# Kernel tuning notes

Measured on AMD Instinct MI355X. Metric: run time of the kernel, lower is better.

Reference implementation:

```python
import jax, jax.numpy as jnp
import numpy as np

EMBED = 1024
HEADS = 16
HEAD_DIM = EMBED // HEADS
SCALE = HEAD_DIM ** -0.5


def setup_inputs() -> dict:
    key = jax.random.key(0)
    ks = jax.random.split(key, 9)
    B, N = 2, 2048
    std = EMBED ** -0.5
    return {
        "query": jax.random.normal(ks[0], (B, N, EMBED), jnp.float32),
        "key": jax.random.normal(ks[1], (B, N, EMBED), jnp.float32),
        "value": jax.random.normal(ks[2], (B, N, EMBED), jnp.float32),
        # torch nn.Linear weights are [out, in]; y = x @ W.T + b
        "Wq": jax.random.normal(ks[3], (EMBED, EMBED), jnp.float32) * std,
        "bq": jax.random.normal(ks[4], (EMBED,), jnp.float32) * 0.01,
        "Wk": jax.random.normal(ks[5], (EMBED, EMBED), jnp.float32) * std,
        "bk": jax.random.normal(ks[6], (EMBED,), jnp.float32) * 0.01,
        "Wv": jax.random.normal(ks[7], (EMBED, EMBED), jnp.float32) * std,
        "bv": jax.random.normal(ks[8], (EMBED,), jnp.float32) * 0.01,
    }


def reference(query, key, value, Wq, bq, Wk, bk, Wv, bv):
    B, NQ, _ = query.shape
    NK = key.shape[1]
    q = query @ Wq.T + bq  # [B, NQ, E]
    k = key @ Wk.T + bk    # [B, NK, E]
    v = value @ Wv.T + bv  # [B, NK, E]
    # split heads -> [B, H, N, Dh]
    q = q.reshape(B, NQ, HEADS, HEAD_DIM).transpose(0, 2, 1, 3)
    k = k.reshape(B, NK, HEADS, HEAD_DIM).transpose(0, 2, 1, 3)
    v = v.reshape(B, NK, HEADS, HEAD_DIM).transpose(0, 2, 1, 3)
    attn = jnp.einsum("bhqd,bhkd->bhqk", q, k) * SCALE  # [B, H, NQ, NK]
    attn = jax.nn.softmax(attn, axis=-1)
    out = jnp.einsum("bhqk,bhkd->bhqd", attn, v)  # [B, H, NQ, Dh]
    out = out.transpose(0, 2, 1, 3).reshape(B, NQ, EMBED)
    # o_proj is Identity (odim == embed_dim, o_proj=False); dropout is 0 (eval)
    return out
```

## Files before the change

### kernel.cpp

```cpp
#include <hip/hip_runtime.h>

#define EMB 1024
#define NSEQ 2048
#define NBATCH 2
#define NHEAD 16
#define DHEAD 64
#define QSCALE 0.18033688011112042f

typedef float f32x4 __attribute__((ext_vector_type(4)));
typedef short s16x8 __attribute__((ext_vector_type(8)));
typedef short s16x4 __attribute__((ext_vector_type(4)));

typedef __attribute__((address_space(3))) short lds_short;
typedef __attribute__((address_space(1))) const short glb_short;

__device__ __forceinline__ void gl_lds16(const short* g, short* l) {
    __builtin_amdgcn_global_load_lds((glb_short*)g, (lds_short*)l, 16, 0, 0);
}

__device__ __forceinline__ short bf16r(float f) {
    unsigned u = __float_as_uint(f);
    u += 0x7fffu + ((u >> 16) & 1u);
    return (short)(u >> 16);
}

__device__ __forceinline__ unsigned pkbf(float a, float b) {
#if defined(__has_builtin) && __has_builtin(__builtin_amdgcn_cvt_pk_bf16_f32)
    auto r = __builtin_amdgcn_cvt_pk_bf16_f32(a, b);
    unsigned u;
    __builtin_memcpy(&u, &r, 4);
    return u;
#else
    return ((unsigned)bf16r(a) & 0xffffu) | ((unsigned)bf16r(b) << 16);
#endif
}

__device__ __forceinline__ float fexp2(float x) {
#if defined(__has_builtin) && __has_builtin(__builtin_amdgcn_exp2f)
    return __builtin_amdgcn_exp2f(x);
#else
    return exp2f(x);
#endif
}

__global__ __launch_bounds__(256) void cvt6_kernel(
    const float* __restrict__ s0, const float* __restrict__ s1, const float* __restrict__ s2,
    const float* __restrict__ s3, const float* __restrict__ s4, const float* __restrict__ s5,
    short* __restrict__ d0, short* __restrict__ d1, short* __restrict__ d2,
    short* __restrict__ d3, short* __restrict__ d4, short* __restrict__ d5,
    int n0, int n1, int n2, int n3, int n4, int n5)
{
    const int seg = blockIdx.y;
    const float* s = (seg == 0) ? s0 : (seg == 1) ? s1 : (seg == 2) ? s2
                   : (seg == 3) ? s3 : (seg == 4) ? s4 : s5;
    short* d = (seg == 0) ? d0 : (seg == 1) ? d1 : (seg == 2) ? d2
             : (seg == 3) ? d3 : (seg == 4) ? d4 : d5;
    const int n = (seg == 0) ? n0 : (seg == 1) ? n1 : (seg == 2) ? n2
                : (seg == 3) ? n3 : (seg == 4) ? n4 : n5;

    const int i = (blockIdx.x * 256 + threadIdx.x) * 8;
    if (i >= n) return;
    float4 a = *(const float4*)(s + i);
    float4 b = *(const float4*)(s + i + 4);
    uint4 u = { pkbf(a.x, a.y), pkbf(a.z, a.w), pkbf(b.x, b.y), pkbf(b.z, b.w) };
    *(uint4*)(d + i) = u;
}

__global__ __launch_bounds__(256, 3) void proj2_kernel(
    const short* __restrict__ Xq, const short* __restrict__ Xk, const short* __restrict__ Xv,
    const short* __restrict__ Wq, const short* __restrict__ Wk, const short* __restrict__ Wv,
    const float* __restrict__ bq, const float* __restrict__ bk, const float* __restrict__ bv,
    short* __restrict__ Oq, short* __restrict__ Ok, short* __restrict__ Ov)
{
    const int z = blockIdx.z;
    const short* X    = (z == 0) ? Xq : (z == 1) ? Xk : Xv;
    const short* W    = (z == 0) ? Wq : (z == 1) ? Wk : Wv;
    const float* bias = (z == 0) ? bq : (z == 1) ? bk : bv;
    short* Out        = (z == 0) ? Oq : (z == 1) ? Ok : Ov;
    const float osc   = (z == 0) ? QSCALE : 1.0f;

    const int n0 = blockIdx.x * 128;
    const int m0 = blockIdx.y * 128;

    __shared__ __align__(16) short As[128 * 64];
    __shared__ __align__(16) short Bs[128 * 64];

    const int t    = threadIdx.x;
    const int lane = t & 63;
    const int wave = t >> 6;
    const int r    = lane & 15;
    const int quad = lane >> 4;
    const int wm   = (wave >> 1) * 64;
    const int wn   = (wave & 1) * 64;

    const int p0    = wave * 256 + lane;
    const int row0  = p0 >> 3;
    const int lc0   = (p0 & 7) ^ (row0 & 7);
    const short* gA = X + (size_t)(m0 + row0) * EMB + lc0 * 8;
    const short* gB = W + (size_t)(n0 + row0) * EMB + lc0 * 8;
    short* lA = As + p0 * 8;
    short* lB = Bs + p0 * 8;

    f32x4 acc[4][4];
#pragma unroll
    for (int i = 0; i < 4; ++i)
#pragma unroll
        for (int j = 0; j < 4; ++j)
#pragma unroll
            for (int v = 0; v < 4; ++v) acc[i][j][v] = 0.f;

    for (int k0 = 0; k0 < EMB; k0 += 64) {
#pragma unroll
        for (int i = 0; i < 4; ++i) {
            gl_lds16(gA + k0 + (size_t)8 * i * EMB, lA + i * 512);
            gl_lds16(gB + k0 + (size_t)8 * i * EMB, lB + i * 512);
        }
        __syncthreads();

#pragma unroll
        for (int ks = 0; ks < 2; ++ks) {
            const int fc = ((ks * 4 + quad) ^ (r & 7)) * 8;
            s16x8 af[4], bf[4];
#pragma unroll
            for (int i = 0; i < 4; ++i) af[i] = *(const s16x8*)&As[(wm + i * 16 + r) * 64 + fc];
#pragma unroll
            for (int j = 0; j < 4; ++j) bf[j] = *(const s16x8*)&Bs[(wn + j * 16 + r) * 64 + fc];
#pragma unroll
            for (int i = 0; i < 4; ++i)
#pragma unroll
                for (int j = 0; j < 4; ++j)
                    acc[i][j] = __builtin_amdgcn_mfma_f32_16x16x32_bf16(af[i], bf[j], acc[i][j], 0, 0, 0);
        }
        __syncthreads();
    }

    if (z != 2) {
#pragma unroll
        for (int j = 0; j < 4; ++j) {
            const int gn = n0 + wn + j * 16 + r;
            const float bb = bias[gn];
#pragma unroll
            for (int i = 0; i < 4; ++i)
#pragma unroll
                for (int reg = 0; reg < 4; ++reg) {
                    const int gm = m0 + wm + i * 16 + quad * 4 + reg;
                    Out[(size_t)gm * EMB + gn] = bf16r((acc[i][j][reg] + bb) * osc);
                }
        }
    } else {
#pragma unroll
        for (int j = 0; j < 4; ++j) {
            const int gn = n0 + wn + j * 16 + r;
            const float bb = bias[gn];
            const int hh = gn >> 6;
            const int dd = gn & 63;
#pragma unroll
            for (int i = 0; i < 4; ++i) {
                const int gm = m0 + wm + i * 16 + quad * 4;
                const int bi = gm >> 11;
                const int nn = gm & 2047;
                s16x4 pk;
#pragma unroll
                for (int reg = 0; reg < 4; ++reg) pk[reg] = bf16r(acc[i][j][reg] + bb);
                *(s16x4*)(Out + ((size_t)(bi * NHEAD + hh) * DHEAD + dd) * NSEQ + nn) = pk;
            }
        }
    }
}

__global__ __launch_bounds__(256) void proj_kernel(
    const float* __restrict__ Xq, const float* __restrict__ Xk, const float* __restrict__ Xv,
    const float* __restrict__ Wq, const float* __restrict__ Wk, const float* __restrict__ Wv,
    const float* __restrict__ bq, const float* __restrict__ bk, const float* __restrict__ bv,
    short* __restrict__ Oq, short* __restrict__ Ok, short* __restrict__ Ov)
{
    const int z = blockIdx.z;
    const float* X    = (z == 0) ? Xq : (z == 1) ? Xk : Xv;
    const float* W    = (z == 0) ? Wq : (z == 1) ? Wk : Wv;
    const float* bias = (z == 0) ? bq : (z == 1) ? bk : bv;
    short* Out        = (z == 0) ? Oq : (z == 1) ? Ok : Ov;
    const float osc   = (z == 0) ? QSCALE : 1.0f;

    const int n0 = blockIdx.x * 128;
    const int m0 = blockIdx.y * 128;

    __shared__ __align__(16) short As[128][40];
    __shared__ __align__(16) short Bs[128][40];

    const int t    = threadIdx.x;
    const int lane = t & 63;
    const int wave = t >> 6;
    const int r    = lane & 15;
    const int quad = lane >> 4;
    const int wm   = (wave >> 1) * 64;
    const int wn   = (wave & 1) * 64;

    const int srow = t >> 1;
    const int scol = (t & 1) << 4;

    f32x4 acc[4][4];
#pragma unroll
    for (int i = 0; i < 4; ++i)
#pragma unroll
        for (int j = 0; j < 4; ++j)
#pragma unroll
            for (int v = 0; v < 4; ++v) acc[i][j][v] = 0.f;

    for (int k0 = 0; k0 < EMB; k0 += 32) {
        const float4* xp = (const float4*)(X + (size_t)(m0 + srow) * EMB + k0 + scol);
        const float4* wp = (const float4*)(W + (size_t)(n0 + srow) * EMB + k0 + scol);
        float4 x0 = xp[0], x1 = xp[1], x2 = xp[2], x3 = xp[3];
        float4 w0 = wp[0], w1 = wp[1], w2 = wp[2], w3 = wp[3];
        uint4 a0 = { pkbf(x0.x, x0.y), pkbf(x0.z, x0.w), pkbf(x1.x, x1.y), pkbf(x1.z, x1.w) };
        uint4 a1 = { pkbf(x2.x, x2.y), pkbf(x2.z, x2.w), pkbf(x3.x, x3.y), pkbf(x3.z, x3.w) };
        uint4 b0 = { pkbf(w0.x, w0.y), pkbf(w0.z, w0.w), pkbf(w1.x, w1.y), pkbf(w1.z, w1.w) };
        uint4 b1 = { pkbf(w2.x, w2.y), pkbf(w2.z, w2.w), pkbf(w3.x, w3.y), pkbf(w3.z, w3.w) };
        *(uint4*)&As[srow][scol]     = a0;
        *(uint4*)&As[srow][scol + 8] = a1;
        *(uint4*)&Bs[srow][scol]     = b0;
        *(uint4*)&Bs[srow][scol + 8] = b1;
        __syncthreads();

        s16x8 af[4], bf[4];
#pragma unroll
        for (int i = 0; i < 4; ++i) af[i] = *(const s16x8*)&As[wm + i * 16 + r][quad * 8];
#pragma unroll
        for (int j = 0; j < 4; ++j) bf[j] = *(const s16x8*)&Bs[wn + j * 16 + r][quad * 8];
#pragma unroll
        for (int i = 0; i < 4; ++i)
#pragma unroll
            for (int j = 0; j < 4; ++j)
                acc[i][j] = __builtin_amdgcn_mfma_f32_16x16x32_bf16(af[i], bf[j], acc[i][j], 0, 0, 0);
        __syncthreads();
    }

#pragma unroll
    for (int j = 0; j < 4; ++j) {
        const int gn = n0 + wn + j * 16 + r;
        const float bb = bias[gn];
#pragma unroll
        for (int i = 0; i < 4; ++i)
#pragma unroll
            for (int reg = 0; reg < 4; ++reg) {
                const int gm = m0 + wm + i * 16 + quad * 4 + reg;
                Out[(size_t)gm * EMB + gn] = bf16r((acc[i][j][reg] + bb) * osc);
            }
    }
}

__global__ __launch_bounds__(256) void vtrans_kernel(
    const short* __restrict__ Vp, short* __restrict__ VT)
{
    const int n0 = blockIdx.x * 64;
    const int h  = blockIdx.y;
    const int b  = blockIdx.z;
    __shared__ __align__(16) short L[64][72];

    const int t  = threadIdx.x;
    const int rr = t >> 2;
    const int cc = (t & 3) * 16;

    const short* src = Vp + (size_t)(b * NSEQ + n0 + rr) * EMB + h * DHEAD + cc;
    s16x8 a = *(const s16x8*)src;
    s16x8 c = *(const s16x8*)(src + 8);
    *(s16x8*)&L[rr][cc]     = a;
    *(s16x8*)&L[rr][cc + 8] = c;
    __syncthreads();

    const int d  = t >> 2;
    const int c4 = (t & 3) * 16;
    short vals[16];
#pragma unroll
    for (int i = 0; i < 16; ++i) vals[i] = L[c4 + i][d];
    short* dst = VT + ((size_t)(b * NHEAD + h) * DHEAD + d) * NSEQ + n0 + c4;
    *(s16x8*)dst       = *(s16x8*)&vals[0];
    *(s16x8*)(dst + 8) = *(s16x8*)&vals[8];
}

__global__ __launch_bounds__(512, 4) void attn8_kernel(
    const short* __restrict__ Qp, const short* __restrict__ Kp,
    const short* __restrict__ VT, float* __restrict__ Out)
{
    const int qblk = blockIdx.x * 128;
    const int h    = blockIdx.y;
    const int b    = blockIdx.z;

    __shared__ __align__(16) char smem[34816];
    short* Ks   = (short*)smem;
    short* Vs   = (short*)smem + 128 * 64;
    float* fbuf = (float*)smem;

    const int t    = threadIdx.x;
    const int lane = t & 63;
    const int w    = t >> 6;
    const int r    = lane & 15;
    const int quad = lane >> 4;
    const int r7   = r & 7;

    const size_t rowbase = (size_t)b * NSEQ;
    const int    colbase = h * DHEAD;
    const size_t bh64    = (size_t)(b * NHEAD + h) * DHEAD;

    const short* qrow = Qp + (rowbase + qblk + w * 16 + r) * EMB + colbase;
    const s16x8 qf0 = *(const s16x8*)(qrow + quad * 8);
    const s16x8 qf1 = *(const s16x8*)(qrow + 32 + quad * 8);

    f32x4 accO[4];
#pragma unroll
    for (int dt = 0; dt < 4; ++dt)
#pragma unroll
        for (int v = 0; v < 4; ++v) accO[dt][v] = 0.f;
    float lsum0 = 0.f, lsum1 = 0.f;
    const f32x4 zf = {0.f, 0.f, 0.f, 0.f};

    const int krow = t >> 2;
    const int kc   = (t & 3) * 2;
    const int kcs  = kc ^ (krow & 7);
    const short* gK = Kp + (rowbase + krow) * EMB + colbase + kc * 8;
    short* lK0 = Ks + krow * 64 + kcs * 8;
    short* lK1 = Ks + krow * 64 + (kcs ^ 1) * 8;

    const int vrow = t >> 3;
    const int vc   = (t & 7) * 2;
    const int vcs  = vc ^ (vrow & 7);
    const short* gV = VT + (bh64 + vrow) * NSEQ + vc * 8;
    short* lV0 = Vs + vrow * 128 + vcs * 8;
    short* lV1 = Vs + vrow * 128 + (vcs ^ 1) * 8;

    const int kofs = (quad ^ r7) * 8;
    int vofs[4];
    {
        const int x4  = r7 & 4;
        const int qr3 = ((quad >> 1) ^ r7) & 3;
#pragma unroll
        for (int s = 0; s < 4; ++s)
            vofs[s] = ((((s << 2) ^ x4) | qr3) * 8) + (quad & 1) * 4;
    }

    s16x8 kr0 = *(const s16x8*)gK;
    s16x8 kr1 = *(const s16x8*)(gK + 8);
    s16x8 vr0 = *(const s16x8*)gV;
    s16x8 vr1 = *(const s16x8*)(gV + 8);
    const short* gKn = gK + (size_t)128 * EMB;
    const short* gVn = gV + 128;

    for (int kt = 0; kt < 16; ++kt) {
        *(s16x8*)lK0 = kr0;
        *(s16x8*)lK1 = kr1;
        *(s16x8*)lV0 = vr0;
        *(s16x8*)lV1 = vr1;
        __syncthreads();

        if (kt + 1 < 16) {
            kr0 = *(const s16x8*)gKn;
            kr1 = *(const s16x8*)(gKn + 8);
            vr0 = *(const s16x8*)gVn;
            vr1 = *(const s16x8*)(gVn + 8);
            gKn += (size_t)128 * EMB;
            gVn += 128;
        }

        s16x8 pf[4];
#pragma unroll
        for (int s = 0; s < 4; ++s) {
            const short* kb = Ks + (s * 32 + r) * 64;
            const s16x8 kf00 = *(const s16x8*)(kb + kofs);
            const s16x8 kf01 = *(const s16x8*)(kb + (kofs ^ 32));
            const s16x8 kf10 = *(const s16x8*)(kb + 16 * 64 + kofs);
            const s16x8 kf11 = *(const s16x8*)(kb + 16 * 64 + (kofs ^ 32));
            __builtin_amdgcn_s_setprio(1);
            f32x4 s0 = __builtin_amdgcn_mfma_f32_16x16x32_bf16(
                kf01, qf1, __builtin_amdgcn_mfma_f32_16x16x32_bf16(kf00, qf0, zf, 0, 0, 0), 0, 0, 0);
            f32x4 s1 = __builtin_amdgcn_mfma_f32_16x16x32_bf16(
                kf11, qf1, __builtin_amdgcn_mfma_f32_16x16x32_bf16(kf10, qf0, zf, 0, 0, 0), 0, 0, 0);
            __builtin_amdgcn_s_setprio(0);
            float p0[4], p1[4];
#pragma unroll
            for (int reg = 0; reg < 4; ++reg) {
                p0[reg] = fexp2(s0[reg]);
                p1[reg] = fexp2(s1[reg]);
                lsum0 += p0[reg];
                lsum1 += p1[reg];
            }
            uint4 uu = { pkbf(p0[0], p0[1]), pkbf(p0[2], p0[3]),
                         pkbf(p1[0], p1[1]), pkbf(p1[2], p1[3]) };
            __builtin_memcpy(&pf[s], &uu, 16);
        }

#pragma unroll
        for (int dt = 0; dt < 4; ++dt) {
            const short* vb = Vs + (dt * 16 + r) * 128;
            s16x8 vfl[4];
#pragma unroll
            for (int s = 0; s < 4; ++s) {
                s16x4 lo = *(const s16x4*)(vb + vofs[s]);
                s16x4 hi = *(const s16x4*)(vb + (vofs[s] ^ 16));
                vfl[s] = __builtin_shufflevector(lo, hi, 0, 1, 2, 3, 4, 5, 6, 7);
            }
            __builtin_amdgcn_s_setprio(1);
#pragma unroll
            for (int s = 0; s < 4; ++s)
                accO[dt] = __builtin_amdgcn_mfma_f32_16x16x32_bf16(vfl[s], pf[s], accO[dt], 0, 0, 0);
            __builtin_amdgcn_s_setprio(0);
        }
        __syncthreads();
    }

    float ls = lsum0 + lsum1;
    ls += __shfl_xor(ls, 16);
    ls += __shfl_xor(ls, 32);
    const float rl = 1.f / ls;

#pragma unroll
    for (int dt = 0; dt < 4; ++dt)
#pragma unroll
        for (int reg = 0; reg < 4; ++reg)
            fbuf[(w * 16 + r) * 68 + dt * 16 + quad * 4 + reg] = accO[dt][reg] * rl;
    __syncthreads();
    const int qi = t >> 2;
    const int c  = (t & 3) * 16;
    const float4* fp = (const float4*)&fbuf[qi * 68 + c];
    float4 o0 = fp[0], o1 = fp[1], o2 = fp[2], o3 = fp[3];
    float* op = Out + (rowbase + qblk + qi) * EMB + colbase + c;
    ((float4*)op)[0] = o0;
    ((float4*)op)[1] = o1;
    ((float4*)op)[2] = o2;
    ((float4*)op)[3] = o3;
}

__global__ __launch_bounds__(256) void attn_fb_kernel(
    const short* __restrict__ Qp, const short* __restrict__ Kp,
    const short* __restrict__ Vp, float* __restrict__ Out)
{
    const int qt = blockIdx.x;
    const int h  = blockIdx.y;
    const int b  = blockIdx.z;

    __shared__ __align__(16) short Ks[64][72];
    __shared__ __align__(16) short VsT[64][72];
    __shared__ __align__(16) short Ps[4][16][72];

    const int t    = threadIdx.x;
    const int lane = t & 63;
    const int w    = t >> 6;
    const int r    = lane & 15;
    const int quad = lane >> 4;

    const size_t rowbase = (size_t)b * NSEQ;
    const int colbase    = h * DHEAD;

    const short* Qr = Qp + (rowbase + qt * 64 + w * 16 + r) * EMB + colbase;
    const s16x8 qf0 = *(const s16x8*)(Qr + quad * 8);
    const s16x8 qf1 = *(const s16x8*)(Qr + 32 + quad * 8);

    float mrow[4], lrow[4];
    f32x4 accO[4];
#pragma unroll
    for (int i = 0; i < 4; ++i) {
        mrow[i] = -INFINITY;
        lrow[i] = 0.f;
#pragma unroll
        for (int v = 0; v < 4; ++v) accO[i][v] = 0.f;
    }

    const int srow = t >> 2;
    const int scol = (t & 3) << 4;

    for (int kt = 0; kt < 32; ++kt) {
        const short* Krow = Kp + (rowbase + kt * 64 + srow) * EMB + colbase + scol;
        const short* Vrow = Vp + (rowbase + kt * 64 + srow) * EMB + colbase + scol;
        s16x8 kv0 = *(const s16x8*)Krow;
        s16x8 kv1 = *(const s16x8*)(Krow + 8);
        s16x8 vv0 = *(const s16x8*)Vrow;
        s16x8 vv1 = *(const s16x8*)(Vrow + 8);
        *(s16x8*)&Ks[srow][scol]     = kv0;
        *(s16x8*)&Ks[srow][scol + 8] = kv1;
#pragma unroll
        for (int i = 0; i < 8; ++i) {
            VsT[scol + i][srow]     = vv0[i];
            VsT[scol + 8 + i][srow] = vv1[i];
        }
        __syncthreads();

        f32x4 sacc[4];
#pragma unroll
        for (int j = 0; j < 4; ++j) {
#pragma unroll
            for (int v = 0; v < 4; ++v) sacc[j][v] = 0.f;
            s16x8 kf0 = *(const s16x8*)&Ks[j * 16 + r][quad * 8];
            s16x8 kf1 = *(const s16x8*)&Ks[j * 16 + r][32 + quad * 8];
            sacc[j] = __builtin_amdgcn_mfma_f32_16x16x32_bf16(qf0, kf0, sacc[j], 0, 0, 0);
            sacc[j] = __builtin_amdgcn_mfma_f32_16x16x32_bf16(qf1, kf1, sacc[j], 0, 0, 0);
        }

        float rmax[4];
#pragma unroll
        for (int reg = 0; reg < 4; ++reg) rmax[reg] = -INFINITY;
#pragma unroll
        for (int j = 0; j < 4; ++j)
#pragma unroll
            for (int reg = 0; reg < 4; ++reg)
                rmax[reg] = fmaxf(rmax[reg], sacc[j][reg]);
#pragma unroll
        for (int reg = 0; reg < 4; ++reg) {
#pragma unroll
            for (int mask = 1; mask <= 8; mask <<= 1)
                rmax[reg] = fmaxf(rmax[reg], __shfl_xor(rmax[reg], mask, 64));
        }

        float alpha[4], rsum[4];
#pragma unroll
        for (int reg = 0; reg < 4; ++reg) {
            float mnew = fmaxf(mrow[reg], rmax[reg]);
            alpha[reg] = fexp2(mrow[reg] - mnew);
            mrow[reg]  = mnew;
            rsum[reg]  = 0.f;
        }

#pragma unroll
        for (int j = 0; j < 4; ++j)
#pragma unroll
            for (int reg = 0; reg < 4; ++reg) {
                float p = fexp2(sacc[j][reg] - mrow[reg]);
                rsum[reg] += p;
                Ps[w][quad * 4 + reg][j * 16 + r] = bf16r(p);
            }
#pragma unroll
        for (int reg = 0; reg < 4; ++reg) {
#pragma unroll
            for (int mask = 1; mask <= 8; mask <<= 1)
                rsum[reg] += __shfl_xor(rsum[reg], mask, 64);
            lrow[reg] = lrow[reg] * alpha[reg] + rsum[reg];
        }
#pragma unroll
        for (int j = 0; j < 4; ++j)
#pragma unroll
            for (int reg = 0; reg < 4; ++reg) accO[j][reg] *= alpha[reg];

#pragma unroll
        for (int s = 0; s < 2; ++s) {
            s16x8 pfr = *(const s16x8*)&Ps[w][r][s * 32 + quad * 8];
#pragma unroll
            for (int j = 0; j < 4; ++j) {
                s16x8 vfr = *(const s16x8*)&VsT[j * 16 + r][s * 32 + quad * 8];
                accO[j] = __builtin_amdgcn_mfma_f32_16x16x32_bf16(pfr, vfr, accO[j], 0, 0, 0);
            }
        }
        __syncthreads();
    }

#pragma unroll
    for (int j = 0; j < 4; ++j)
#pragma unroll
        for (int reg = 0; reg < 4; ++reg) {
            const int qrow = qt * 64 + w * 16 + quad * 4 + reg;
            Out[(rowbase + qrow) * EMB + colbase + j * 16 + r] = accO[j][reg] / lrow[reg];
        }
}

extern "C" void kernel_launch(void* const* d_in, const int* in_sizes, int n_in,
                              void* d_out, int out_size, void* d_ws, size_t ws_size,
                              hipStream_t stream) {
    const float* query = (const float*)d_in[0];
    const float* key   = (const float*)d_in[1];
    const float* value = (const float*)d_in[2];
    const float* Wq    = (const float*)d_in[3];
    const float* bq    = (const float*)d_in[4];
    const float* Wk    = (const float*)d_in[5];
    const float* bk    = (const float*)d_in[6];
    const float* Wv    = (const float*)d_in[7];
    const float* bv    = (const float*)d_in[8];
    float* out = (float*)d_out;

    const size_t XBUF = (size_t)NBATCH * NSEQ * EMB;
    const size_t WBUF = (size_t)EMB * EMB;

    short* Qb  = (short*)d_ws;
    short* Kb  = Qb + XBUF;
    short* Vb  = Kb + XBUF;
    short* VTb = Vb + XBUF;
    short* Xqb = VTb + XBUF;
    short* Xkb = Xqb + XBUF;
    short* Xvb = Xkb + XBUF;
    short* Wqb = Xvb + XBUF;
    short* Wkb = Wqb + WBUF;
    short* Wvb = Wkb + WBUF;

    const size_t need_full  = (7 * XBUF + 3 * WBUF) * sizeof(short);
    const size_t need_attn8 = 4 * XBUF * sizeof(short);

    if (ws_size >= need_full) {
        cvt6_kernel<<<dim3(2048, 6), 256, 0, stream>>>(
            query, key, value, Wq, Wk, Wv,
            Xqb, Xkb, Xvb, Wqb, Wkb, Wvb,
            (int)XBUF, (int)XBUF, (int)XBUF, (int)WBUF, (int)WBUF, (int)WBUF);
        proj2_kernel<<<dim3(EMB / 128, (NBATCH * NSEQ) / 128, 3), 256, 0, stream>>>(
            Xqb, Xkb, Xvb, Wqb, Wkb, Wvb, bq, bk, bv, Qb, Kb, VTb);
        attn8_kernel<<<dim3(NSEQ / 128, NHEAD, NBATCH), 512, 0, stream>>>(Qb, Kb, VTb, out);
    } else if (ws_size >= need_attn8) {
        proj_kernel<<<dim3(EMB / 128, (NBATCH * NSEQ) / 128, 3), 256, 0, stream>>>(
            query, key, value, Wq, Wk, Wv, bq, bk, bv, Qb, Kb, Vb);
        vtrans_kernel<<<dim3(NSEQ / 64, NHEAD, NBATCH), 256, 0, stream>>>(Vb, VTb);
        attn8_kernel<<<dim3(NSEQ / 128, NHEAD, NBATCH), 512, 0, stream>>>(Qb, Kb, VTb, out);
    } else {
        proj_kernel<<<dim3(EMB / 128, (NBATCH * NSEQ) / 128, 3), 256, 0, stream>>>(
            query, key, value, Wq, Wk, Wv, bq, bk, bv, Qb, Kb, Vb);
        attn_fb_kernel<<<dim3(NSEQ / 64, NHEAD, NBATCH), 256, 0, stream>>>(Qb, Kb, Vb, out);
    }
}
```

Measured before the change: 207.7 us.

## Split attention waves into two KV groups with 32-row query strips

The 8 waves are split into two groups, each handling half of a 256-key tile while every wave now computes 32 query rows instead of 16. The kernel loops 8 times over 256-key tiles instead of 16 times over 128-key tiles, halving the barriers and letting each K/V fragment read from LDS feed two query strips. The two groups' partial outputs and row sums are merged through shared memory at the end. In exchange, LDS use grows to 64KB and register pressure rises from doubled accumulators, which may reduce occupancy.

New measurement: 298.1 us. +43.5%, slower.

```diff
diff --git a/kernel.cpp b/kernel.cpp
--- a/kernel.cpp
+++ b/kernel.cpp
@@ -277,7 +277,7 @@
     *(s16x8*)(dst + 8) = *(s16x8*)&vals[8];
 }
 
-__global__ __launch_bounds__(512, 4) void attn8_kernel(
+__global__ __launch_bounds__(512, 4) void attn9_kernel(
     const short* __restrict__ Qp, const short* __restrict__ Kp,
     const short* __restrict__ VT, float* __restrict__ Out)
 {
@@ -285,48 +285,58 @@
     const int h    = blockIdx.y;
     const int b    = blockIdx.z;
 
-    __shared__ __align__(16) char smem[34816];
-    short* Ks   = (short*)smem;
-    short* Vs   = (short*)smem + 128 * 64;
-    float* fbuf = (float*)smem;
-
-    const int t    = threadIdx.x;
-    const int lane = t & 63;
-    const int w    = t >> 6;
-    const int r    = lane & 15;
-    const int quad = lane >> 4;
-    const int r7   = r & 7;
+    __shared__ __align__(16) char smem[65536];
+    short* KsBase = (short*)smem;
+    short* VsBase = (short*)smem + 16384;
+    float* fbuf   = (float*)smem;
+
+    const int t     = threadIdx.x;
+    const int lane  = t & 63;
+    const int w     = t >> 6;
+    const int g     = w >> 2;
+    const int strip = w & 3;
+    const int r     = lane & 15;
+    const int quad  = lane >> 4;
+    const int r7    = r & 7;
 
     const size_t rowbase = (size_t)b * NSEQ;
     const int    colbase = h * DHEAD;
     const size_t bh64    = (size_t)(b * NHEAD + h) * DHEAD;
 
-    const short* qrow = Qp + (rowbase + qblk + w * 16 + r) * EMB + colbase;
-    const s16x8 qf0 = *(const s16x8*)(qrow + quad * 8);
-    const s16x8 qf1 = *(const s16x8*)(qrow + 32 + quad * 8);
-
-    f32x4 accO[4];
-#pragma unroll
-    for (int dt = 0; dt < 4; ++dt)
-#pragma unroll
-        for (int v = 0; v < 4; ++v) accO[dt][v] = 0.f;
-    float lsum0 = 0.f, lsum1 = 0.f;
+    s16x8 qf[2][2];
+#pragma unroll
+    for (int qs = 0; qs < 2; ++qs)
+#pragma unroll
+        for (int ks = 0; ks < 2; ++ks)
+            qf[qs][ks] = *(const s16x8*)(Qp + (rowbase + qblk + strip * 32 + qs * 16 + r) * EMB
+                                          + colbase + ks * 32 + quad * 8);
+
+    f32x4 accO[2][4];
+#pragma unroll
+    for (int qs = 0; qs < 2; ++qs)
+#pragma unroll
+        for (int dt = 0; dt < 4; ++dt)
+#pragma unroll
+            for (int v = 0; v < 4; ++v) accO[qs][dt][v] = 0.f;
+    float lsum[2] = {0.f, 0.f};
     const f32x4 zf = {0.f, 0.f, 0.f, 0.f};
 
     const int krow = t >> 2;
     const int kc   = (t & 3) * 2;
     const int kcs  = kc ^ (krow & 7);
     const short* gK = Kp + (rowbase + krow) * EMB + colbase + kc * 8;
-    short* lK0 = Ks + krow * 64 + kcs * 8;
-    short* lK1 = Ks + krow * 64 + (kcs ^ 1) * 8;
+    short* lK0 = KsBase + krow * 64 + kcs * 8;
+    short* lK1 = KsBase + krow * 64 + (kcs ^ 1) * 8;
 
     const int vrow = t >> 3;
     const int vc   = (t & 7) * 2;
     const int vcs  = vc ^ (vrow & 7);
     const short* gV = VT + (bh64 + vrow) * NSEQ + vc * 8;
-    short* lV0 = Vs + vrow * 128 + vcs * 8;
-    short* lV1 = Vs + vrow * 128 + (vcs ^ 1) * 8;
-
+    short* lV0 = VsBase + vrow * 128 + vcs * 8;
+    short* lV1 = VsBase + vrow * 128 + (vcs ^ 1) * 8;
+
+    const short* Ksg = KsBase + g * 8192;
+    const short* Vsg = VsBase + g * 8192;
     const int kofs = (quad ^ r7) * 8;
     int vofs[4];
     {
@@ -337,59 +347,71 @@
             vofs[s] = ((((s << 2) ^ x4) | qr3) * 8) + (quad & 1) * 4;
     }
 
-    s16x8 kr0 = *(const s16x8*)gK;
-    s16x8 kr1 = *(const s16x8*)(gK + 8);
-    s16x8 vr0 = *(const s16x8*)gV;
-    s16x8 vr1 = *(const s16x8*)(gV + 8);
-    const short* gKn = gK + (size_t)128 * EMB;
-    const short* gVn = gV + 128;
-
-    for (int kt = 0; kt < 16; ++kt) {
-        *(s16x8*)lK0 = kr0;
-        *(s16x8*)lK1 = kr1;
-        *(s16x8*)lV0 = vr0;
-        *(s16x8*)lV1 = vr1;
-        __syncthreads();
-
-        if (kt + 1 < 16) {
-            kr0 = *(const s16x8*)gKn;
-            kr1 = *(const s16x8*)(gKn + 8);
-            vr0 = *(const s16x8*)gVn;
-            vr1 = *(const s16x8*)(gVn + 8);
-            gKn += (size_t)128 * EMB;
-            gVn += 128;
-        }
-
-        s16x8 pf[4];
+    s16x8 ka0 = *(const s16x8*)gK;
+    s16x8 ka1 = *(const s16x8*)(gK + 8);
+    s16x8 kb0 = *(const s16x8*)(gK + (size_t)128 * EMB);
+    s16x8 kb1 = *(const s16x8*)(gK + (size_t)128 * EMB + 8);
+    s16x8 va0 = *(const s16x8*)gV;
+    s16x8 va1 = *(const s16x8*)(gV + 8);
+    s16x8 vb0 = *(const s16x8*)(gV + 128);
+    s16x8 vb1 = *(const s16x8*)(gV + 136);
+
+    for (int it = 0; it < 8; ++it) {
+        *(s16x8*)lK0 = ka0;
+        *(s16x8*)lK1 = ka1;
+        *(s16x8*)(lK0 + 8192) = kb0;
+        *(s16x8*)(lK1 + 8192) = kb1;
+        *(s16x8*)lV0 = va0;
+        *(s16x8*)lV1 = va1;
+        *(s16x8*)(lV0 + 8192) = vb0;
+        *(s16x8*)(lV1 + 8192) = vb1;
+        __syncthreads();
+
+        if (it + 1 < 8) {
+            const short* gKi = gK + (size_t)(it + 1) * 256 * EMB;
+            const short* gVi = gV + (it + 1) * 256;
+            ka0 = *(const s16x8*)gKi;
+            ka1 = *(const s16x8*)(gKi + 8);
+            kb0 = *(const s16x8*)(gKi + (size_t)128 * EMB);
+            kb1 = *(const s16x8*)(gKi + (size_t)128 * EMB + 8);
+            va0 = *(const s16x8*)gVi;
+            va1 = *(const s16x8*)(gVi + 8);
+            vb0 = *(const s16x8*)(gVi + 128);
+            vb1 = *(const s16x8*)(gVi + 136);
+        }
+
+        s16x8 pf[2][4];
 #pragma unroll
         for (int s = 0; s < 4; ++s) {
-            const short* kb = Ks + (s * 32 + r) * 64;
+            const short* kb = Ksg + (s * 32 + r) * 64;
             const s16x8 kf00 = *(const s16x8*)(kb + kofs);
             const s16x8 kf01 = *(const s16x8*)(kb + (kofs ^ 32));
-            const s16x8 kf10 = *(const s16x8*)(kb + 16 * 64 + kofs);
-            const s16x8 kf11 = *(const s16x8*)(kb + 16 * 64 + (kofs ^ 32));
-            __builtin_amdgcn_s_setprio(1);
-            f32x4 s0 = __builtin_amdgcn_mfma_f32_16x16x32_bf16(
-                kf01, qf1, __builtin_amdgcn_mfma_f32_16x16x32_bf16(kf00, qf0, zf, 0, 0, 0), 0, 0, 0);
-            f32x4 s1 = __builtin_amdgcn_mfma_f32_16x16x32_bf16(
-                kf11, qf1, __builtin_amdgcn_mfma_f32_16x16x32_bf16(kf10, qf0, zf, 0, 0, 0), 0, 0, 0);
-            __builtin_amdgcn_s_setprio(0);
-            float p0[4], p1[4];
-#pragma unroll
-            for (int reg = 0; reg < 4; ++reg) {
-                p0[reg] = fexp2(s0[reg]);
-                p1[reg] = fexp2(s1[reg]);
-                lsum0 += p0[reg];
-                lsum1 += p1[reg];
+            const s16x8 kf10 = *(const s16x8*)(kb + 1024 + kofs);
+            const s16x8 kf11 = *(const s16x8*)(kb + 1024 + (kofs ^ 32));
+#pragma unroll
+            for (int qs = 0; qs < 2; ++qs) {
+                __builtin_amdgcn_s_setprio(1);
+                f32x4 s0 = __builtin_amdgcn_mfma_f32_16x16x32_bf16(
+                    kf01, qf[qs][1], __builtin_amdgcn_mfma_f32_16x16x32_bf16(kf00, qf[qs][0], zf, 0, 0, 0), 0, 0, 0);
+                f32x4 s1 = __builtin_amdgcn_mfma_f32_16x16x32_bf16(
+                    kf11, qf[qs][1], __builtin_amdgcn_mfma_f32_16x16x32_bf16(kf10, qf[qs][0], zf, 0, 0, 0), 0, 0, 0);
+                __builtin_amdgcn_s_setprio(0);
+                float p0[4], p1[4];
+#pragma unroll
+                for (int reg = 0; reg < 4; ++reg) {
+                    p0[reg] = fexp2(s0[reg]);
+                    p1[reg] = fexp2(s1[reg]);
+                    lsum[qs] += p0[reg] + p1[reg];
+                }
+                uint4 uu = { pkbf(p0[0], p0[1]), pkbf(p0[2], p0[3]),
+                             pkbf(p1[0], p1[1]), pkbf(p1[2], p1[3]) };
+                __builtin_memcpy(&pf[qs][s], &uu, 16);
             }
-            uint4 uu = { pkbf(p0[0], p0[1]), pkbf(p0[2], p0[3]),
-                         pkbf(p1[0], p1[1]), pkbf(p1[2], p1[3]) };
-            __builtin_memcpy(&pf[s], &uu, 16);
         }
 
 #pragma unroll
         for (int dt = 0; dt < 4; ++dt) {
-            const short* vb = Vs + (dt * 16 + r) * 128;
+            const short* vb = Vsg + (dt * 16 + r) * 128;
             s16x8 vfl[4];
 #pragma unroll
             for (int s = 0; s < 4; ++s) {
@@ -399,24 +421,52 @@
             }
             __builtin_amdgcn_s_setprio(1);
 #pragma unroll
-            for (int s = 0; s < 4; ++s)
-                accO[dt] = __builtin_amdgcn_mfma_f32_16x16x32_bf16(vfl[s], pf[s], accO[dt], 0, 0, 0);
+            for (int qs = 0; qs < 2; ++qs)
+#pragma unroll
+                for (int s = 0; s < 4; ++s)
+                    accO[qs][dt] = __builtin_amdgcn_mfma_f32_16x16x32_bf16(vfl[s], pf[qs][s], accO[qs][dt], 0, 0, 0);
             __builtin_amdgcn_s_setprio(0);
         }
         __syncthreads();
     }
 
-    float ls = lsum0 + lsum1;
-    ls += __shfl_xor(ls, 16);
-    ls += __shfl_xor(ls, 32);
-    const float rl = 1.f / ls;
-
-#pragma unroll
-    for (int dt = 0; dt < 4; ++dt)
-#pragma unroll
-        for (int reg = 0; reg < 4; ++reg)
-            fbuf[(w * 16 + r) * 68 + dt * 16 + quad * 4 + reg] = accO[dt][reg] * rl;
+    if (g == 1) {
+#pragma unroll
+        for (int qs = 0; qs < 2; ++qs) {
+            const int q = strip * 32 + qs * 16 + r;
+#pragma unroll
+            for (int dt = 0; dt < 4; ++dt)
+#pragma unroll
+                for (int reg = 0; reg < 4; ++reg)
+                    fbuf[q * 68 + dt * 16 + quad * 4 + reg] = accO[qs][dt][reg];
+            fbuf[q * 68 + 64 + quad] = lsum[qs];
+        }
+    }
     __syncthreads();
+    if (g == 0) {
+        float rl[2];
+#pragma unroll
+        for (int qs = 0; qs < 2; ++qs) {
+            const int q = strip * 32 + qs * 16 + r;
+            float s = lsum[qs] + fbuf[q * 68 + 64 + quad];
+            s += __shfl_xor(s, 16);
+            s += __shfl_xor(s, 32);
+            rl[qs] = 1.f / s;
+        }
+#pragma unroll
+        for (int qs = 0; qs < 2; ++qs) {
+            const int q = strip * 32 + qs * 16 + r;
+#pragma unroll
+            for (int dt = 0; dt < 4; ++dt)
+#pragma unroll
+                for (int reg = 0; reg < 4; ++reg) {
+                    const int idx = q * 68 + dt * 16 + quad * 4 + reg;
+                    fbuf[idx] = (accO[qs][dt][reg] + fbuf[idx]) * rl[qs];
+                }
+        }
+    }
+    __syncthreads();
+
     const int qi = t >> 2;
     const int c  = (t & 3) * 16;
     const float4* fp = (const float4*)&fbuf[qi * 68 + c];
@@ -587,7 +637,7 @@
     short* Wvb = Wkb + WBUF;
 
     const size_t need_full  = (7 * XBUF + 3 * WBUF) * sizeof(short);
-    const size_t need_attn8 = 4 * XBUF * sizeof(short);
+    const size_t need_attn9 = 4 * XBUF * sizeof(short);
 
     if (ws_size >= need_full) {
         cvt6_kernel<<<dim3(2048, 6), 256, 0, stream>>>(
@@ -596,12 +646,12 @@
             (int)XBUF, (int)XBUF, (int)XBUF, (int)WBUF, (int)WBUF, (int)WBUF);
         proj2_kernel<<<dim3(EMB / 128, (NBATCH * NSEQ) / 128, 3), 256, 0, stream>>>(
             Xqb, Xkb, Xvb, Wqb, Wkb, Wvb, bq, bk, bv, Qb, Kb, VTb);
-        attn8_kernel<<<dim3(NSEQ / 128, NHEAD, NBATCH), 512, 0, stream>>>(Qb, Kb, VTb, out);
-    } else if (ws_size >= need_attn8) {
+        attn9_kernel<<<dim3(NSEQ / 128, NHEAD, NBATCH), 512, 0, stream>>>(Qb, Kb, VTb, out);
+    } else if (ws_size >= need_attn9) {
         proj_kernel<<<dim3(EMB / 128, (NBATCH * NSEQ) / 128, 3), 256, 0, stream>>>(
             query, key, value, Wq, Wk, Wv, bq, bk, bv, Qb, Kb, Vb);
         vtrans_kernel<<<dim3(NSEQ / 64, NHEAD, NBATCH), 256, 0, stream>>>(Vb, VTb);
-        attn8_kernel<<<dim3(NSEQ / 128, NHEAD, NBATCH), 512, 0, stream>>>(Qb, Kb, VTb, out);
+        attn9_kernel<<<dim3(NSEQ / 128, NHEAD, NBATCH), 512, 0, stream>>>(Qb, Kb, VTb, out);
     } else {
         proj_kernel<<<dim3(EMB / 128, (NBATCH * NSEQ) / 128, 3), 256, 0, stream>>>(
             query, key, value, Wq, Wk, Wv, bq, bk, bv, Qb, Kb, Vb);
```
